# Performance work log

Measured on AMD Instinct MI355X. Metric: run time of the kernel, lower is better.

The kernel has to match this reference:

```python
import jax, jax.numpy as jnp
import numpy as np

HIDDEN = 256


def _lstm_cell(x, h, c, W_ih, W_hh, b_ih, b_hh):
    # torch.nn.LSTMCell: gates ordered [i, f, g, o], gates = x W_ih^T + h W_hh^T + b_ih + b_hh
    gates = x @ W_ih.T + h @ W_hh.T + (b_ih + b_hh)
    i, f, g, o = jnp.split(gates, 4, axis=-1)
    c_new = jax.nn.sigmoid(f) * c + jax.nn.sigmoid(i) * jnp.tanh(g)
    h_new = jax.nn.sigmoid(o) * jnp.tanh(c_new)
    return h_new, c_new


def setup_inputs() -> dict:
    key = jax.random.key(0)
    ks = jax.random.split(key, 16)
    s = 1.0 / np.sqrt(HIDDEN)  # torch LSTMCell init scale
    inp = {
        "tracks": jax.random.normal(ks[0], (256, 512, 2), dtype=jnp.float32),
        "W_ih0": jax.random.uniform(ks[1], (1024, 2), jnp.float32, -s, s),
        "W_hh0": jax.random.uniform(ks[2], (1024, 256), jnp.float32, -s, s),
        "b_ih0": jax.random.uniform(ks[3], (1024,), jnp.float32, -s, s),
        "b_hh0": jax.random.uniform(ks[4], (1024,), jnp.float32, -s, s),
        "W_ih1": jax.random.uniform(ks[5], (1024, 256), jnp.float32, -s, s),
        "W_hh1": jax.random.uniform(ks[6], (1024, 256), jnp.float32, -s, s),
        "b_ih1": jax.random.uniform(ks[7], (1024,), jnp.float32, -s, s),
        "b_hh1": jax.random.uniform(ks[8], (1024,), jnp.float32, -s, s),
        "W_ih2": jax.random.uniform(ks[9], (1024, 256), jnp.float32, -s, s),
        "W_hh2": jax.random.uniform(ks[10], (1024, 256), jnp.float32, -s, s),
        "b_ih2": jax.random.uniform(ks[11], (1024,), jnp.float32, -s, s),
        "b_hh2": jax.random.uniform(ks[12], (1024,), jnp.float32, -s, s),
        "W_pred": jax.random.uniform(ks[13], (2, 256), jnp.float32, -s, s),
        "b_pred": jax.random.uniform(ks[14], (2,), jnp.float32, -s, s),
    }
    return inp


def reference(tracks, W_ih0, W_hh0, b_ih0, b_hh0, W_ih1, W_hh1, b_ih1, b_hh1,
              W_ih2, W_hh2, b_ih2, b_hh2, W_pred, b_pred):
    B = tracks.shape[0]
    layers = [(W_ih0, W_hh0, b_ih0, b_hh0),
              (W_ih1, W_hh1, b_ih1, b_hh1),
              (W_ih2, W_hh2, b_ih2, b_hh2)]
    zeros = jnp.zeros((B, HIDDEN), dtype=tracks.dtype)
    init_carry = tuple((zeros, zeros) for _ in layers)

    def step(carry, x_t):
        new_carry = []
        h = x_t
        for (hc, params) in zip(carry, layers):
            h, c = _lstm_cell(h, hc[0], hc[1], *params)
            new_carry.append((h, c))
        return tuple(new_carry), None

    xs = jnp.swapaxes(tracks, 0, 1)  # [T, B, 2]
    final_carry, _ = jax.lax.scan(step, init_carry, xs)
    h = final_carry[-1][0]  # last layer's final hidden state
    h = jax.nn.elu(h)
    return h @ W_pred.T + b_pred
```

## Files before the change

### kernel.cpp

```cpp
#include <hip/hip_runtime.h>
#include <math.h>

typedef __attribute__((ext_vector_type(4))) float f32x4;
typedef __attribute__((ext_vector_type(4))) int   i32x4;
typedef __attribute__((ext_vector_type(8))) short bfrag8;

#define WRE_LO_OFF 2621440
#define HB_OFF     5242880
#define FLAGS_OFF  6029312

#define WROW 264
#define SMEM_BYTES (4 * 64 * WROW * 2)

__device__ __forceinline__ unsigned short f2bf(float f){
  union { float f; unsigned u; } x; x.f = f;
  unsigned r = x.u + 0x7FFFu + ((x.u >> 16) & 1u);
  return (unsigned short)(r >> 16);
}
__device__ __forceinline__ float bf2f(unsigned short s){
  union { unsigned u; float f; } x; x.u = ((unsigned)s) << 16; return x.f;
}
__device__ __forceinline__ float sigf(float x){
  return 1.0f / (1.0f + __expf(-x));
}
__device__ __forceinline__ float tanh_fast(float x){
  x = fminf(fmaxf(x, -15.0f), 15.0f);
  float e = __expf(2.0f * x);
  return (e - 1.0f) / (e + 1.0f);
}

__device__ __forceinline__ i32x4 llc_load_b128(const void* p){
  i32x4 r;
  asm volatile("global_load_dwordx4 %0, %1, off sc0 sc1"
               : "=v"(r) : "v"(p) : "memory");
  return r;
}
__device__ __forceinline__ void llc_store_b16(void* p, unsigned short v){
  unsigned int vv = v;
  asm volatile("global_store_short %0, %1, off sc0 sc1"
               : : "v"(p), "v"(vv) : "memory");
}
__device__ __forceinline__ void wait_vm0(){
  asm volatile("s_waitcnt vmcnt(0)" ::: "memory");
}

__global__ void init_reorder(const float* __restrict__ hh0, const float* __restrict__ ih1,
                             const float* __restrict__ hh1, const float* __restrict__ ih2,
                             const float* __restrict__ hh2,
                             unsigned short* __restrict__ wre_hi,
                             unsigned short* __restrict__ wre_lo){
  int e = blockIdx.x * 256 + threadIdx.x;
  int mat = e >> 18;
  int d   = (e >> 8) & 1023;
  int k   = e & 255;
  int nt = d >> 6, g = (d >> 4) & 3, n = d & 15;
  int src_row = g*256 + nt*16 + n;
  const float* W = (mat==0) ? hh0 : (mat==1) ? ih1 : (mat==2) ? hh1 : (mat==3) ? ih2 : hh2;
  float v = W[src_row*256 + k];
  unsigned short hi = f2bf(v);
  float lo = v - bf2f(hi);
  wre_hi[e] = hi;
  wre_lo[e] = f2bf(lo);
}

__global__ void init_zero(uint4* __restrict__ p, int n16){
  int i = blockIdx.x * 256 + threadIdx.x;
  if (i < n16) p[i] = make_uint4(0u,0u,0u,0u);
}

__global__ void lstm_coop(
    const float* __restrict__ tracks,
    const float* __restrict__ wih0,
    const float* __restrict__ bih0, const float* __restrict__ bhh0,
    const float* __restrict__ bih1, const float* __restrict__ bhh1,
    const float* __restrict__ bih2, const float* __restrict__ bhh2,
    const unsigned short* __restrict__ wre_hi, const unsigned short* __restrict__ wre_lo,
    unsigned short* __restrict__ hb, unsigned int* __restrict__ flags)
{
  extern __shared__ __align__(16) unsigned short smem[];

  const int tid  = threadIdx.x;
  const int l    = blockIdx.x >> 6;
  const int r6   = blockIdx.x & 63;
  const int nt   = r6 & 15, bt = r6 >> 4;
  const int b0   = bt * 64, n0 = nt * 16;
  const int w    = tid >> 6, lane = tid & 63;
  const int m    = lane & 15, q = lane >> 4;

  unsigned int* colflags = flags + bt * 1024;
  unsigned int* mycnt    = colflags + nt * 64;

  const int nmats = (l == 0) ? 1 : 2;
  const int gmat0 = (l == 0) ? 0 : (l == 1 ? 1 : 3);
  for (int mi = 0; mi < nmats; ++mi){
    const unsigned short* sh = wre_hi + (gmat0 + mi)*262144 + nt*16384;
    const unsigned short* sl = wre_lo + (gmat0 + mi)*262144 + nt*16384;
    unsigned short* dh = smem + (mi*2 + 0)*64*WROW;
    unsigned short* dl = smem + (mi*2 + 1)*64*WROW;
    for (int c = tid; c < 2048; c += 256){
      int r = c >> 5, off = (c & 31) * 8;
      *(uint4*)(dh + r*WROW + off) = *(const uint4*)(sh + r*256 + off);
      *(uint4*)(dl + r*WROW + off) = *(const uint4*)(sl + r*256 + off);
    }
  }
  __syncthreads();

  const float* bihL = (l==0) ? bih0 : (l==1) ? bih1 : bih2;
  const float* bhhL = (l==0) ? bhh0 : (l==1) ? bhh1 : bhh2;
  float bsum[4], wx[4][2];
  #pragma unroll
  for (int g = 0; g < 4; ++g){
    int row = g*256 + n0 + m;
    bsum[g] = bihL[row] + bhhL[row];
    wx[g][0] = wih0[row*2 + 0];
    wx[g][1] = wih0[row*2 + 1];
  }
  float cst[4] = {0.f, 0.f, 0.f, 0.f};
  const int arow = b0 + 16*w + m;
  const int woff = m*WROW + q*8;

  for (int s = 0; s < 514; ++s){
    const int t = s - l;
    const bool active = (t >= 0) && (t < 512);

    float xv0[4], xv1[4];
    if (l == 0 && active){
      #pragma unroll
      for (int r = 0; r < 4; ++r){
        const float* px = tracks + (b0 + 16*w + q*4 + r)*1024 + t*2;
        xv0[r] = px[0]; xv1[r] = px[1];
      }
    }

    if (s > 0){
      if (tid < 64){
        const unsigned int tgt = 3u * (unsigned)s;
        for (;;){
          unsigned int v = tgt;
          if (tid < 16)
            v = __hip_atomic_load(colflags + tid*64, __ATOMIC_RELAXED,
                                  __HIP_MEMORY_SCOPE_AGENT);
          if (__all((int)(v >= tgt))) break;
          __builtin_amdgcn_s_sleep(1);
        }
      }
      __syncthreads();
    }

    if (active){
      const int pt = t & 1, pp = pt ^ 1;

      i32x4 ar_raw[8], ai_raw[8];
      {
        const unsigned short* prec = hb + ((pp*3 + l)*256 + arow)*256 + q*8;
        #pragma unroll
        for (int ks = 0; ks < 8; ++ks)
          ar_raw[ks] = llc_load_b128(prec + ks*32);
        if (l >= 1){
          const unsigned short* pin = hb + ((pt*3 + (l-1))*256 + arow)*256 + q*8;
          #pragma unroll
          for (int ks = 0; ks < 8; ++ks)
            ai_raw[ks] = llc_load_b128(pin + ks*32);
        }
      }
      wait_vm0();

      f32x4 acc[4];
      #pragma unroll
      for (int g = 0; g < 4; ++g) acc[g] = (f32x4){0.f,0.f,0.f,0.f};

      {
        const unsigned short* bh = smem + ((l==0?0:2) + 0)*64*WROW + woff;
        const unsigned short* bl = smem + ((l==0?0:2) + 1)*64*WROW + woff;
        #pragma unroll
        for (int ks = 0; ks < 8; ++ks){
          bfrag8 a = __builtin_bit_cast(bfrag8, ar_raw[ks]);
          #pragma unroll
          for (int g = 0; g < 4; ++g){
            bfrag8 fh = *(const bfrag8*)(bh + g*16*WROW + ks*32);
            bfrag8 fl = *(const bfrag8*)(bl + g*16*WROW + ks*32);
            acc[g] = __builtin_amdgcn_mfma_f32_16x16x32_bf16(a, fh, acc[g], 0, 0, 0);
            acc[g] = __builtin_amdgcn_mfma_f32_16x16x32_bf16(a, fl, acc[g], 0, 0, 0);
          }
        }
      }
      if (l >= 1){
        const unsigned short* bh = smem + 0*64*WROW + woff;
        const unsigned short* bl = smem + 1*64*WROW + woff;
        #pragma unroll
        for (int ks = 0; ks < 8; ++ks){
          bfrag8 a = __builtin_bit_cast(bfrag8, ai_raw[ks]);
          #pragma unroll
          for (int g = 0; g < 4; ++g){
            bfrag8 fh = *(const bfrag8*)(bh + g*16*WROW + ks*32);
            bfrag8 fl = *(const bfrag8*)(bl + g*16*WROW + ks*32);
            acc[g] = __builtin_amdgcn_mfma_f32_16x16x32_bf16(a, fh, acc[g], 0, 0, 0);
            acc[g] = __builtin_amdgcn_mfma_f32_16x16x32_bf16(a, fl, acc[g], 0, 0, 0);
          }
        }
      }

      unsigned short* hout = hb + ((pt*3 + l)*256 + 0)*256;
      #pragma unroll
      for (int r = 0; r < 4; ++r){
        float xi = 0.f, xf = 0.f, xg = 0.f, xo = 0.f;
        if (l == 0){
          xi = xv0[r]*wx[0][0] + xv1[r]*wx[0][1];
          xf = xv0[r]*wx[1][0] + xv1[r]*wx[1][1];
          xg = xv0[r]*wx[2][0] + xv1[r]*wx[2][1];
          xo = xv0[r]*wx[3][0] + xv1[r]*wx[3][1];
        }
        float gi = acc[0][r] + bsum[0] + xi;
        float gf = acc[1][r] + bsum[1] + xf;
        float gg = acc[2][r] + bsum[2] + xg;
        float go = acc[3][r] + bsum[3] + xo;
        float iv = sigf(gi);
        float fv = sigf(gf);
        float gv = tanh_fast(gg);
        float ov = sigf(go);
        cst[r] = fv * cst[r] + iv * gv;
        float hv = ov * tanh_fast(cst[r]);
        llc_store_b16(&hout[(b0 + 16*w + q*4 + r)*256 + n0 + m], f2bf(hv));
      }
    }

    wait_vm0();
    __syncthreads();
    if (tid == 0)
      __hip_atomic_fetch_add(mycnt, 1u, __ATOMIC_RELAXED, __HIP_MEMORY_SCOPE_AGENT);
  }
}

__global__ void head_kernel(const unsigned short* __restrict__ hb,
                            const float* __restrict__ wpred,
                            const float* __restrict__ bpred,
                            float* __restrict__ out){
  const int b = blockIdx.x;
  const int k = threadIdx.x;
  const int idx = (5*256 + b)*256 + k;
  float h = bf2f(hb[idx]);
  float e = (h > 0.f) ? h : expm1f(h);
  float v0 = e * wpred[k];
  float v1 = e * wpred[256 + k];
  #pragma unroll
  for (int off = 32; off > 0; off >>= 1){
    v0 += __shfl_down(v0, off, 64);
    v1 += __shfl_down(v1, off, 64);
  }
  __shared__ float r0[4], r1[4];
  int wv = threadIdx.x >> 6, ln = threadIdx.x & 63;
  if (ln == 0){ r0[wv] = v0; r1[wv] = v1; }
  __syncthreads();
  if (threadIdx.x == 0){
    out[b*2 + 0] = r0[0] + r0[1] + r0[2] + r0[3] + bpred[0];
    out[b*2 + 1] = r1[0] + r1[1] + r1[2] + r1[3] + bpred[1];
  }
}

extern "C" void kernel_launch(void* const* d_in, const int* in_sizes, int n_in,
                              void* d_out, int out_size, void* d_ws, size_t ws_size,
                              hipStream_t stream) {
  const float* tracks = (const float*)d_in[0];
  const float* wih0   = (const float*)d_in[1];
  const float* whh0   = (const float*)d_in[2];
  const float* bih0   = (const float*)d_in[3];
  const float* bhh0   = (const float*)d_in[4];
  const float* wih1   = (const float*)d_in[5];
  const float* whh1   = (const float*)d_in[6];
  const float* bih1   = (const float*)d_in[7];
  const float* bhh1   = (const float*)d_in[8];
  const float* wih2   = (const float*)d_in[9];
  const float* whh2   = (const float*)d_in[10];
  const float* bih2   = (const float*)d_in[11];
  const float* bhh2   = (const float*)d_in[12];
  const float* wpred  = (const float*)d_in[13];
  const float* bpred  = (const float*)d_in[14];
  float* out = (float*)d_out;

  char* ws = (char*)d_ws;
  unsigned short* wre_hi = (unsigned short*)(ws);
  unsigned short* wre_lo = (unsigned short*)(ws + WRE_LO_OFF);
  unsigned short* hb     = (unsigned short*)(ws + HB_OFF);
  unsigned int*   flags  = (unsigned int*)(ws + FLAGS_OFF);

  (void)hipFuncSetAttribute((const void*)lstm_coop,
                            hipFuncAttributeMaxDynamicSharedMemorySize, SMEM_BYTES);

  init_reorder<<<5120, 256, 0, stream>>>(whh0, wih1, whh1, wih2, whh2, wre_hi, wre_lo);
  init_zero<<<197, 256, 0, stream>>>((uint4*)(ws + HB_OFF), 50176);

  void* args[12];
  args[0]  = (void*)&tracks;
  args[1]  = (void*)&wih0;
  args[2]  = (void*)&bih0;
  args[3]  = (void*)&bhh0;
  args[4]  = (void*)&bih1;
  args[5]  = (void*)&bhh1;
  args[6]  = (void*)&bih2;
  args[7]  = (void*)&bhh2;
  args[8]  = (void*)&wre_hi;
  args[9]  = (void*)&wre_lo;
  args[10] = (void*)&hb;
  args[11] = (void*)&flags;
  hipLaunchCooperativeKernel((const void*)lstm_coop, dim3(192), dim3(256), args,
                             SMEM_BYTES, stream);

  head_kernel<<<256, 256, 0, stream>>>(hb, wpred, bpred, out);
}
```

Baseline: 3.383 ms.

## Replace lockstep block barriers with per-wave dataflow tags and 4-deep h buffers

Replaces the global per-step counter barrier, in which every layer advanced in lockstep with a block-wide __syncthreads, with per-wave tag flags. Each wave waits only on the 16 column tiles of its own 16 batch rows, for the previous layer's input and its own recurrent state. The hidden-state ring grows from 2 to 4 slots, and a write-after-read guard lets layers run up to several steps apart. The per-layer loop is templated to drop runtime layer branches, and the sleep in the spin loop is removed. This adds more busy polling traffic and more complex ordering logic.

```diff
diff --git a/kernel.cpp b/kernel.cpp
--- a/kernel.cpp
+++ b/kernel.cpp
@@ -7,7 +7,8 @@
 
 #define WRE_LO_OFF 2621440
 #define HB_OFF     5242880
-#define FLAGS_OFF  6029312
+#define TAG_OFF    6815744
+#define HSTRIDE    65536
 
 #define WROW 264
 #define SMEM_BYTES (4 * 64 * WROW * 2)
@@ -68,27 +69,187 @@
   if (i < n16) p[i] = make_uint4(0u,0u,0u,0u);
 }
 
-__global__ void lstm_coop(
+__global__ void init_tags(unsigned int* __restrict__ tags){
+  int i = blockIdx.x * 256 + threadIdx.x;
+  if (i < 3072) tags[i] = (unsigned)(i / 768);
+}
+
+__global__ void __launch_bounds__(256, 1) lstm_coop(
     const float* __restrict__ tracks,
     const float* __restrict__ wih0,
     const float* __restrict__ bih0, const float* __restrict__ bhh0,
     const float* __restrict__ bih1, const float* __restrict__ bhh1,
     const float* __restrict__ bih2, const float* __restrict__ bhh2,
     const unsigned short* __restrict__ wre_hi, const unsigned short* __restrict__ wre_lo,
-    unsigned short* __restrict__ hb, unsigned int* __restrict__ flags)
+    unsigned short* __restrict__ hb, unsigned int* __restrict__ tags);
+
+template<int L>
+__device__ __forceinline__ void layer_loop(
+    const float* __restrict__ tracks, const float* __restrict__ wih0,
+    const float* __restrict__ bihL, const float* __restrict__ bhhL,
+    const unsigned short* smem,
+    unsigned short* hb, unsigned int* tags,
+    int nt, int bt)
+{
+  const int tid  = threadIdx.x;
+  const int w    = tid >> 6, lane = tid & 63;
+  const int m    = lane & 15, q = lane >> 4;
+  const int b0   = bt * 64, n0 = nt * 16;
+  const int G    = bt * 4 + w;
+
+  float bsum[4], wx0[4], wx1[4];
+  #pragma unroll
+  for (int g = 0; g < 4; ++g){
+    int row = g*256 + n0 + m;
+    bsum[g] = bihL[row] + bhhL[row];
+    if constexpr (L == 0){ wx0[g] = wih0[row*2 + 0]; wx1[g] = wih0[row*2 + 1]; }
+  }
+  float cst[4] = {0.f, 0.f, 0.f, 0.f};
+  const int arow = b0 + 16*w + m;
+  const int woff = m*WROW + q*8;
+  constexpr int RS = (L == 0) ? 0 : 2;
+
+  for (int t = 0; t < 512; ++t){
+    const int pin  = t & 3;
+    const int prec = (t + 3) & 3;
+    const unsigned expi = (unsigned)(t + 4);
+    const unsigned expr = (unsigned)(t + 3);
+
+    unsigned gv = 0u;
+    unsigned int* gl = nullptr;
+    if constexpr (L < 2){
+      gl = tags + ((pin*3 + (L+1))*16 + G)*16;
+      if (lane < 16)
+        gv = __hip_atomic_load(gl + lane, __ATOMIC_RELAXED, __HIP_MEMORY_SCOPE_AGENT);
+    }
+
+    float xv0[4], xv1[4];
+    if constexpr (L == 0){
+      #pragma unroll
+      for (int r = 0; r < 4; ++r){
+        const float* px = tracks + (b0 + 16*w + q*4 + r)*1024 + t*2;
+        xv0[r] = px[0]; xv1[r] = px[1];
+      }
+    }
+
+    unsigned int* rcl = tags + ((prec*3 + L)*16 + G)*16;
+    unsigned int* inl = nullptr;
+    if constexpr (L >= 1) inl = tags + ((pin*3 + (L-1))*16 + G)*16;
+    for (;;){
+      bool ok = true;
+      if constexpr (L >= 1){
+        if (lane < 16)
+          ok = __hip_atomic_load(inl + lane, __ATOMIC_RELAXED, __HIP_MEMORY_SCOPE_AGENT) >= expi;
+        else if (lane < 32)
+          ok = __hip_atomic_load(rcl + (lane - 16), __ATOMIC_RELAXED, __HIP_MEMORY_SCOPE_AGENT) >= expr;
+      } else {
+        if (lane < 16)
+          ok = __hip_atomic_load(rcl + lane, __ATOMIC_RELAXED, __HIP_MEMORY_SCOPE_AGENT) >= expr;
+      }
+      if (__all((int)ok)) break;
+    }
+
+    i32x4 arr[8], ari[8];
+    {
+      const unsigned short* pr = hb + (prec*3 + L)*HSTRIDE + arow*256 + q*8;
+      #pragma unroll
+      for (int ks = 0; ks < 8; ++ks) arr[ks] = llc_load_b128(pr + ks*32);
+      if constexpr (L >= 1){
+        const unsigned short* pi = hb + (pin*3 + (L-1))*HSTRIDE + arow*256 + q*8;
+        #pragma unroll
+        for (int ks = 0; ks < 8; ++ks) ari[ks] = llc_load_b128(pi + ks*32);
+      }
+    }
+    wait_vm0();
+
+    f32x4 acc[4];
+    #pragma unroll
+    for (int g = 0; g < 4; ++g) acc[g] = (f32x4){0.f,0.f,0.f,0.f};
+    {
+      const unsigned short* bh = smem + (RS + 0)*64*WROW + woff;
+      const unsigned short* bl = smem + (RS + 1)*64*WROW + woff;
+      #pragma unroll
+      for (int ks = 0; ks < 8; ++ks){
+        bfrag8 a = __builtin_bit_cast(bfrag8, arr[ks]);
+        #pragma unroll
+        for (int g = 0; g < 4; ++g){
+          bfrag8 fh = *(const bfrag8*)(bh + g*16*WROW + ks*32);
+          bfrag8 fl = *(const bfrag8*)(bl + g*16*WROW + ks*32);
+          acc[g] = __builtin_amdgcn_mfma_f32_16x16x32_bf16(a, fh, acc[g], 0, 0, 0);
+          acc[g] = __builtin_amdgcn_mfma_f32_16x16x32_bf16(a, fl, acc[g], 0, 0, 0);
+        }
+      }
+    }
+    if constexpr (L >= 1){
+      const unsigned short* bh = smem + 0*64*WROW + woff;
+      const unsigned short* bl = smem + 1*64*WROW + woff;
+      #pragma unroll
+      for (int ks = 0; ks < 8; ++ks){
+        bfrag8 a = __builtin_bit_cast(bfrag8, ari[ks]);
+        #pragma unroll
+        for (int g = 0; g < 4; ++g){
+          bfrag8 fh = *(const bfrag8*)(bh + g*16*WROW + ks*32);
+          bfrag8 fl = *(const bfrag8*)(bl + g*16*WROW + ks*32);
+          acc[g] = __builtin_amdgcn_mfma_f32_16x16x32_bf16(a, fh, acc[g], 0, 0, 0);
+          acc[g] = __builtin_amdgcn_mfma_f32_16x16x32_bf16(a, fl, acc[g], 0, 0, 0);
+        }
+      }
+    }
+
+    if constexpr (L < 2){
+      for (;;){
+        bool ok = (lane < 16) ? (gv >= (unsigned)t) : true;
+        if (__all((int)ok)) break;
+        if (lane < 16)
+          gv = __hip_atomic_load(gl + lane, __ATOMIC_RELAXED, __HIP_MEMORY_SCOPE_AGENT);
+      }
+    }
+
+    unsigned short* hout = hb + (pin*3 + L)*HSTRIDE;
+    #pragma unroll
+    for (int r = 0; r < 4; ++r){
+      float xi = 0.f, xf = 0.f, xg = 0.f, xo = 0.f;
+      if constexpr (L == 0){
+        xi = xv0[r]*wx0[0] + xv1[r]*wx1[0];
+        xf = xv0[r]*wx0[1] + xv1[r]*wx1[1];
+        xg = xv0[r]*wx0[2] + xv1[r]*wx1[2];
+        xo = xv0[r]*wx0[3] + xv1[r]*wx1[3];
+      }
+      float gi = acc[0][r] + bsum[0] + xi;
+      float gf = acc[1][r] + bsum[1] + xf;
+      float gg = acc[2][r] + bsum[2] + xg;
+      float go = acc[3][r] + bsum[3] + xo;
+      float iv = sigf(gi);
+      float fv = sigf(gf);
+      float gvv = tanh_fast(gg);
+      float ov = sigf(go);
+      cst[r] = fv * cst[r] + iv * gvv;
+      float hv = ov * tanh_fast(cst[r]);
+      llc_store_b16(&hout[(b0 + 16*w + q*4 + r)*256 + n0 + m], f2bf(hv));
+    }
+
+    wait_vm0();
+    if (lane == 0)
+      __hip_atomic_store(tags + ((pin*3 + L)*16 + G)*16 + nt, (unsigned)(t + 4),
+                         __ATOMIC_RELAXED, __HIP_MEMORY_SCOPE_AGENT);
+  }
+}
+
+__global__ void __launch_bounds__(256, 1) lstm_coop(
+    const float* __restrict__ tracks,
+    const float* __restrict__ wih0,
+    const float* __restrict__ bih0, const float* __restrict__ bhh0,
+    const float* __restrict__ bih1, const float* __restrict__ bhh1,
+    const float* __restrict__ bih2, const float* __restrict__ bhh2,
+    const unsigned short* __restrict__ wre_hi, const unsigned short* __restrict__ wre_lo,
+    unsigned short* __restrict__ hb, unsigned int* __restrict__ tags)
 {
   extern __shared__ __align__(16) unsigned short smem[];
 
-  const int tid  = threadIdx.x;
-  const int l    = blockIdx.x >> 6;
-  const int r6   = blockIdx.x & 63;
-  const int nt   = r6 & 15, bt = r6 >> 4;
-  const int b0   = bt * 64, n0 = nt * 16;
-  const int w    = tid >> 6, lane = tid & 63;
-  const int m    = lane & 15, q = lane >> 4;
-
-  unsigned int* colflags = flags + bt * 1024;
-  unsigned int* mycnt    = colflags + nt * 64;
+  const int tid = threadIdx.x;
+  const int l   = blockIdx.x >> 6;
+  const int r6  = blockIdx.x & 63;
+  const int nt  = r6 & 15, bt = r6 >> 4;
 
   const int nmats = (l == 0) ? 1 : 2;
   const int gmat0 = (l == 0) ? 0 : (l == 1 ? 1 : 3);
@@ -105,130 +266,9 @@
   }
   __syncthreads();
 
-  const float* bihL = (l==0) ? bih0 : (l==1) ? bih1 : bih2;
-  const float* bhhL = (l==0) ? bhh0 : (l==1) ? bhh1 : bhh2;
-  float bsum[4], wx[4][2];
-  #pragma unroll
-  for (int g = 0; g < 4; ++g){
-    int row = g*256 + n0 + m;
-    bsum[g] = bihL[row] + bhhL[row];
-    wx[g][0] = wih0[row*2 + 0];
-    wx[g][1] = wih0[row*2 + 1];
-  }
-  float cst[4] = {0.f, 0.f, 0.f, 0.f};
-  const int arow = b0 + 16*w + m;
-  const int woff = m*WROW + q*8;
-
-  for (int s = 0; s < 514; ++s){
-    const int t = s - l;
-    const bool active = (t >= 0) && (t < 512);
-
-    float xv0[4], xv1[4];
-    if (l == 0 && active){
-      #pragma unroll
-      for (int r = 0; r < 4; ++r){
-        const float* px = tracks + (b0 + 16*w + q*4 + r)*1024 + t*2;
-        xv0[r] = px[0]; xv1[r] = px[1];
-      }
-    }
-
-    if (s > 0){
-      if (tid < 64){
-        const unsigned int tgt = 3u * (unsigned)s;
-        for (;;){
-          unsigned int v = tgt;
-          if (tid < 16)
-            v = __hip_atomic_load(colflags + tid*64, __ATOMIC_RELAXED,
-                                  __HIP_MEMORY_SCOPE_AGENT);
-          if (__all((int)(v >= tgt))) break;
-          __builtin_amdgcn_s_sleep(1);
-        }
-      }
-      __syncthreads();
-    }
-
-    if (active){
-      const int pt = t & 1, pp = pt ^ 1;
-
-      i32x4 ar_raw[8], ai_raw[8];
-      {
-        const unsigned short* prec = hb + ((pp*3 + l)*256 + arow)*256 + q*8;
-        #pragma unroll
-        for (int ks = 0; ks < 8; ++ks)
-          ar_raw[ks] = llc_load_b128(prec + ks*32);
-        if (l >= 1){
-          const unsigned short* pin = hb + ((pt*3 + (l-1))*256 + arow)*256 + q*8;
-          #pragma unroll
-          for (int ks = 0; ks < 8; ++ks)
-            ai_raw[ks] = llc_load_b128(pin + ks*32);
-        }
-      }
-      wait_vm0();
-
-      f32x4 acc[4];
-      #pragma unroll
-      for (int g = 0; g < 4; ++g) acc[g] = (f32x4){0.f,0.f,0.f,0.f};
-
-      {
-        const unsigned short* bh = smem + ((l==0?0:2) + 0)*64*WROW + woff;
-        const unsigned short* bl = smem + ((l==0?0:2) + 1)*64*WROW + woff;
-        #pragma unroll
-        for (int ks = 0; ks < 8; ++ks){
-          bfrag8 a = __builtin_bit_cast(bfrag8, ar_raw[ks]);
-          #pragma unroll
-          for (int g = 0; g < 4; ++g){
-            bfrag8 fh = *(const bfrag8*)(bh + g*16*WROW + ks*32);
-            bfrag8 fl = *(const bfrag8*)(bl + g*16*WROW + ks*32);
-            acc[g] = __builtin_amdgcn_mfma_f32_16x16x32_bf16(a, fh, acc[g], 0, 0, 0);
-            acc[g] = __builtin_amdgcn_mfma_f32_16x16x32_bf16(a, fl, acc[g], 0, 0, 0);
-          }
-        }
-      }
-      if (l >= 1){
-        const unsigned short* bh = smem + 0*64*WROW + woff;
-        const unsigned short* bl = smem + 1*64*WROW + woff;
-        #pragma unroll
-        for (int ks = 0; ks < 8; ++ks){
-          bfrag8 a = __builtin_bit_cast(bfrag8, ai_raw[ks]);
-          #pragma unroll
-          for (int g = 0; g < 4; ++g){
-            bfrag8 fh = *(const bfrag8*)(bh + g*16*WROW + ks*32);
-            bfrag8 fl = *(const bfrag8*)(bl + g*16*WROW + ks*32);
-            acc[g] = __builtin_amdgcn_mfma_f32_16x16x32_bf16(a, fh, acc[g], 0, 0, 0);
-            acc[g] = __builtin_amdgcn_mfma_f32_16x16x32_bf16(a, fl, acc[g], 0, 0, 0);
-          }
-        }
-      }
-
-      unsigned short* hout = hb + ((pt*3 + l)*256 + 0)*256;
-      #pragma unroll
-      for (int r = 0; r < 4; ++r){
-        float xi = 0.f, xf = 0.f, xg = 0.f, xo = 0.f;
-        if (l == 0){
-          xi = xv0[r]*wx[0][0] + xv1[r]*wx[0][1];
-          xf = xv0[r]*wx[1][0] + xv1[r]*wx[1][1];
-          xg = xv0[r]*wx[2][0] + xv1[r]*wx[2][1];
-          xo = xv0[r]*wx[3][0] + xv1[r]*wx[3][1];
-        }
-        float gi = acc[0][r] + bsum[0] + xi;
-        float gf = acc[1][r] + bsum[1] + xf;
-        float gg = acc[2][r] + bsum[2] + xg;
-        float go = acc[3][r] + bsum[3] + xo;
-        float iv = sigf(gi);
-        float fv = sigf(gf);
-        float gv = tanh_fast(gg);
-        float ov = sigf(go);
-        cst[r] = fv * cst[r] + iv * gv;
-        float hv = ov * tanh_fast(cst[r]);
-        llc_store_b16(&hout[(b0 + 16*w + q*4 + r)*256 + n0 + m], f2bf(hv));
-      }
-    }
-
-    wait_vm0();
-    __syncthreads();
-    if (tid == 0)
-      __hip_atomic_fetch_add(mycnt, 1u, __ATOMIC_RELAXED, __HIP_MEMORY_SCOPE_AGENT);
-  }
+  if (l == 0)      layer_loop<0>(tracks, wih0, bih0, bhh0, smem, hb, tags, nt, bt);
+  else if (l == 1) layer_loop<1>(tracks, wih0, bih1, bhh1, smem, hb, tags, nt, bt);
+  else             layer_loop<2>(tracks, wih0, bih2, bhh2, smem, hb, tags, nt, bt);
 }
 
 __global__ void head_kernel(const unsigned short* __restrict__ hb,
@@ -237,7 +277,7 @@
                             float* __restrict__ out){
   const int b = blockIdx.x;
   const int k = threadIdx.x;
-  const int idx = (5*256 + b)*256 + k;
+  const int idx = 11*HSTRIDE + b*256 + k;
   float h = bf2f(hb[idx]);
   float e = (h > 0.f) ? h : expm1f(h);
   float v0 = e * wpred[k];
@@ -281,13 +321,14 @@
   unsigned short* wre_hi = (unsigned short*)(ws);
   unsigned short* wre_lo = (unsigned short*)(ws + WRE_LO_OFF);
   unsigned short* hb     = (unsigned short*)(ws + HB_OFF);
-  unsigned int*   flags  = (unsigned int*)(ws + FLAGS_OFF);
+  unsigned int*   tags   = (unsigned int*)(ws + TAG_OFF);
 
   (void)hipFuncSetAttribute((const void*)lstm_coop,
                             hipFuncAttributeMaxDynamicSharedMemorySize, SMEM_BYTES);
 
   init_reorder<<<5120, 256, 0, stream>>>(whh0, wih1, whh1, wih2, whh2, wre_hi, wre_lo);
-  init_zero<<<197, 256, 0, stream>>>((uint4*)(ws + HB_OFF), 50176);
+  init_zero<<<384, 256, 0, stream>>>((uint4*)(ws + HB_OFF), 98304);
+  init_tags<<<12, 256, 0, stream>>>(tags);
 
   void* args[12];
   args[0]  = (void*)&tracks;
@@ -301,7 +342,7 @@
   args[8]  = (void*)&wre_hi;
   args[9]  = (void*)&wre_lo;
   args[10] = (void*)&hb;
-  args[11] = (void*)&flags;
+  args[11] = (void*)&tags;
   hipLaunchCooperativeKernel((const void*)lstm_coop, dim3(192), dim3(256), args,
                              SMEM_BYTES, stream);
 
```

After: 3.902 ms. +15.3%, slower.
